# Kernel tuning notes

Hardware: AMD Instinct MI355X
Metric: run time of the kernel (lower is better)

## Reference

```python
import jax, jax.numpy as jnp
import numpy as np

M, K, N = 32768, 2048, 2048  # tokens, in_features, out_features
QMIN, QMAX = -128, 127


def setup_inputs() -> dict:
    key = jax.random.key(0)
    ks = jax.random.split(key, 7)
    x = jax.random.normal(ks[0], (M, K), dtype=jnp.float32).astype(jnp.float16)
    int_weight = jax.random.randint(ks[1], (N, K), QMIN, QMAX + 1, dtype=jnp.int32).astype(jnp.int8)
    # calibrated-looking asymmetric activation quant params (fp16 buffers, [num_steps]=1)
    act_delta = (jax.random.uniform(ks[2], (1,), dtype=jnp.float32) * 0.02 + 0.005).astype(jnp.float16)
    act_zp = jnp.round(jax.random.normal(ks[3], (1,), dtype=jnp.float32) * 8.0).astype(jnp.float16)
    # per-output-channel weight scales; fuse precomputed dequant buffers consistently
    w_delta = jax.random.uniform(ks[4], (N,), dtype=jnp.float32) * 0.002 + 1e-4
    act_times_weight_delta = (act_delta.astype(jnp.float32) * w_delta)[None, :]  # [1, N]
    w_row_sum = jnp.sum(int_weight.astype(jnp.float32), axis=1)  # [N]
    zp_times_weight_channel_sum = (act_zp.astype(jnp.float32) * w_row_sum * act_times_weight_delta[0])[None, :]  # [1, N]
    bias = jax.random.normal(ks[5], (N,), dtype=jnp.float32) * 0.02
    return {
        "input": x,
        "act_delta": act_delta,
        "act_zp": act_zp,
        "zp_times_weight_channel_sum": zp_times_weight_channel_sum,
        "act_times_weight_delta": act_times_weight_delta,
        "bias": bias,
        "int_weight": int_weight,
    }


def reference(input, act_delta, act_zp, zp_times_weight_channel_sum,
              act_times_weight_delta, bias, int_weight):
    # current_step == num_steps - 1 == 0
    delta = act_delta[0].astype(jnp.float32)
    zp = act_zp[0].astype(jnp.float32)
    atwd = act_times_weight_delta[0]            # [N] = act_delta * weight_delta
    zp_sum = zp_times_weight_channel_sum[0]     # [N] = zp * rowsum(W_int) * atwd
    # asymmetric int8 activation quantization: q = clip(round(x/delta + zp))
    q = jnp.clip(jnp.round(input.astype(jnp.float32) / delta + zp), QMIN, QMAX).astype(jnp.int8)
    # int8 GEMM with int32 accumulation: [M,K] x [K,N]
    acc = jnp.matmul(q.astype(jnp.int32), int_weight.astype(jnp.int32).T)
    # fused dequant + zero-point correction + bias, cast to fp16
    out = acc.astype(jnp.float32) * atwd - zp_sum + bias
    return out.astype(jnp.float16)
```

## Files before the change

### kernel.cpp

```cpp
#include <hip/hip_runtime.h>
#include <hip/hip_fp16.h>
#include <stdint.h>

typedef int i32x4 __attribute__((ext_vector_type(4)));

#define TM 128
#define TN 128
#define BK 64

__device__ __forceinline__ void gload_lds16(const void* g, void* l) {
  __builtin_amdgcn_global_load_lds(
      (const __attribute__((address_space(1))) unsigned int*)g,
      (__attribute__((address_space(3))) unsigned int*)l, 16, 0, 0);
}

__global__ __launch_bounds__(256) void quant_x_kernel(
    const float* __restrict__ x, const float* __restrict__ deltap,
    const float* __restrict__ zpp, int8_t* __restrict__ q, int n16) {
  int i = blockIdx.x * blockDim.x + threadIdx.x;
  if (i >= n16) return;
  const float delta = deltap[0];
  const float zp = zpp[0];
  const float4* src = (const float4*)x + (size_t)i * 4;
  int packed[4];
#pragma unroll
  for (int g = 0; g < 4; ++g) {
    float4 v = src[g];
    float f0 = fminf(127.f, fmaxf(-128.f, rintf(v.x / delta + zp)));
    float f1 = fminf(127.f, fmaxf(-128.f, rintf(v.y / delta + zp)));
    float f2 = fminf(127.f, fmaxf(-128.f, rintf(v.z / delta + zp)));
    float f3 = fminf(127.f, fmaxf(-128.f, rintf(v.w / delta + zp)));
    int q0 = (int)f0 & 255, q1 = (int)f1 & 255, q2 = (int)f2 & 255, q3 = (int)f3 & 255;
    packed[g] = q0 | (q1 << 8) | (q2 << 16) | (q3 << 24);
  }
  ((int4*)q)[i] = make_int4(packed[0], packed[1], packed[2], packed[3]);
}

__global__ __launch_bounds__(256) void pack_w_kernel(
    const int* __restrict__ w, int8_t* __restrict__ wp, int n16) {
  int i = blockIdx.x * blockDim.x + threadIdx.x;
  if (i >= n16) return;
  const int4* src = (const int4*)w + (size_t)i * 4;
  int packed[4];
#pragma unroll
  for (int g = 0; g < 4; ++g) {
    int4 v = src[g];
    packed[g] = (v.x & 255) | ((v.y & 255) << 8) | ((v.z & 255) << 16) | ((v.w & 255) << 24);
  }
  ((int4*)wp)[i] = make_int4(packed[0], packed[1], packed[2], packed[3]);
}

__global__ __launch_bounds__(256) void gemm_i8_kernel(
    const int8_t* __restrict__ Aq, const int8_t* __restrict__ Bw,
    const float* __restrict__ atwd, const float* __restrict__ zpws,
    const float* __restrict__ bias, float* __restrict__ out,
    int Mc, int Nc, int Kc) {
  __shared__ int8_t sA[TM * BK];
  __shared__ int8_t sB[TN * BK];
  const int bm = blockIdx.y;
  const int bn = blockIdx.x;
  const int t = threadIdx.x;
  const int lane = t & 63;
  const int wave = t >> 6;
  const int wr = wave >> 1;
  const int wc = wave & 1;
  const int fr = lane & 15;
  const int kc = lane >> 4;
  const size_t K = (size_t)Kc;

  i32x4 acc[4][4] = {};

  const int srow = t >> 2;
  const int scol = (t & 3) << 4;
  const int8_t* gA = Aq + (size_t)(bm * TM + srow) * K + scol;
  const int8_t* gB = Bw + (size_t)(bn * TN + srow) * K + scol;
  int8_t* lA = &sA[t * 16];
  int8_t* lB = &sB[t * 16];
  const size_t rowoff = (size_t)64 * K;

  for (int k0 = 0; k0 < Kc; k0 += BK) {
    gload_lds16(gA + k0, lA);
    gload_lds16(gA + k0 + rowoff, lA + 64 * BK);
    gload_lds16(gB + k0, lB);
    gload_lds16(gB + k0 + rowoff, lB + 64 * BK);
    __syncthreads();

    i32x4 af[4], bf[4];
#pragma unroll
    for (int i = 0; i < 4; ++i)
      af[i] = *(const i32x4*)&sA[(wr * 64 + i * 16 + fr) * BK + kc * 16];
#pragma unroll
    for (int j = 0; j < 4; ++j)
      bf[j] = *(const i32x4*)&sB[(wc * 64 + j * 16 + fr) * BK + kc * 16];

#pragma unroll
    for (int i = 0; i < 4; ++i)
#pragma unroll
      for (int j = 0; j < 4; ++j)
        acc[i][j] = __builtin_amdgcn_mfma_i32_16x16x64_i8(af[i], bf[j], acc[i][j], 0, 0, 0);

    __syncthreads();
  }

  const int r4 = (lane >> 4) << 2;
#pragma unroll
  for (int j = 0; j < 4; ++j) {
    const int cn = bn * TN + wc * 64 + j * 16 + fr;
    const float aw = atwd[cn];
    const float zs = zpws[cn];
    const float bs = bias[cn];
#pragma unroll
    for (int i = 0; i < 4; ++i) {
      const size_t rbase = (size_t)(bm * TM + wr * 64 + i * 16 + r4) * (size_t)Nc;
#pragma unroll
      for (int r = 0; r < 4; ++r) {
        float v = (float)acc[i][j][r] * aw - zs + bs;
        v = __half2float(__float2half(v));
        out[rbase + (size_t)r * Nc + cn] = v;
      }
    }
  }
}

extern "C" void kernel_launch(void* const* d_in, const int* in_sizes, int n_in,
                              void* d_out, int out_size, void* d_ws, size_t ws_size,
                              hipStream_t stream) {
  const float* x         = (const float*)d_in[0];
  const float* act_delta = (const float*)d_in[1];
  const float* act_zp    = (const float*)d_in[2];
  const float* zpws      = (const float*)d_in[3];
  const float* atwd      = (const float*)d_in[4];
  const float* bias      = (const float*)d_in[5];
  const int*   w32       = (const int*)d_in[6];
  float* out = (float*)d_out;

  const int N = in_sizes[5];
  const int K = in_sizes[6] / N;
  const int M = in_sizes[0] / K;

  int8_t* q  = (int8_t*)d_ws;
  int8_t* wp = q + (size_t)M * K;

  {
    int n16 = (M * K) / 16;
    quant_x_kernel<<<(n16 + 255) / 256, 256, 0, stream>>>(x, act_delta, act_zp, q, n16);
  }
  {
    int n16 = (N * K) / 16;
    pack_w_kernel<<<(n16 + 255) / 256, 256, 0, stream>>>(w32, wp, n16);
  }
  {
    dim3 grid(N / TN, M / TM);
    gemm_i8_kernel<<<grid, 256, 0, stream>>>(q, wp, atwd, zpws, bias, out, M, N, K);
  }
}
```

Before: 302.7 us.

## Rebuild int8 GEMM with 256x256 tiles, 4-slot LDS pipeline and swizzle

The GEMM moves from 128x128 tiles with a single LDS buffer to 256x256 tiles on 512 threads. A 4-slot LDS ring prefetches three K-steps ahead with explicit vmcnt waits, and MFMA phases are interleaved with the A and B staging. The change also adds an XOR swizzle on LDS columns to avoid bank conflicts, a 1D grid remapped for cache locality, and a reciprocal-multiply in the quantization kernel. The aim is to hide global-load latency and raise data reuse per tile. The cost is 128KB of LDS per block, which limits occupancy, plus hand-tuned wait counts that assume a particular load ordering.

New measurement: 271.1 us. 10.4% less time.

```diff
diff --git a/kernel.cpp b/kernel.cpp
--- a/kernel.cpp
+++ b/kernel.cpp
@@ -4,9 +4,12 @@
 
 typedef int i32x4 __attribute__((ext_vector_type(4)));
 
-#define TM 128
-#define TN 128
-#define BK 64
+#define BM 256
+#define BN 256
+#define BKB 64
+#define NSLOT 4
+#define SLOT_BYTES 32768
+#define THREADS 512
 
 __device__ __forceinline__ void gload_lds16(const void* g, void* l) {
   __builtin_amdgcn_global_load_lds(
@@ -19,17 +22,17 @@
     const float* __restrict__ zpp, int8_t* __restrict__ q, int n16) {
   int i = blockIdx.x * blockDim.x + threadIdx.x;
   if (i >= n16) return;
-  const float delta = deltap[0];
+  const float rdelta = 1.0f / deltap[0];
   const float zp = zpp[0];
   const float4* src = (const float4*)x + (size_t)i * 4;
   int packed[4];
 #pragma unroll
   for (int g = 0; g < 4; ++g) {
     float4 v = src[g];
-    float f0 = fminf(127.f, fmaxf(-128.f, rintf(v.x / delta + zp)));
-    float f1 = fminf(127.f, fmaxf(-128.f, rintf(v.y / delta + zp)));
-    float f2 = fminf(127.f, fmaxf(-128.f, rintf(v.z / delta + zp)));
-    float f3 = fminf(127.f, fmaxf(-128.f, rintf(v.w / delta + zp)));
+    float f0 = fminf(127.f, fmaxf(-128.f, rintf(fmaf(v.x, rdelta, zp))));
+    float f1 = fminf(127.f, fmaxf(-128.f, rintf(fmaf(v.y, rdelta, zp))));
+    float f2 = fminf(127.f, fmaxf(-128.f, rintf(fmaf(v.z, rdelta, zp))));
+    float f3 = fminf(127.f, fmaxf(-128.f, rintf(fmaf(v.w, rdelta, zp))));
     int q0 = (int)f0 & 255, q1 = (int)f1 & 255, q2 = (int)f2 & 255, q3 = (int)f3 & 255;
     packed[g] = q0 | (q1 << 8) | (q2 << 16) | (q3 << 24);
   }
@@ -50,71 +53,115 @@
   ((int4*)wp)[i] = make_int4(packed[0], packed[1], packed[2], packed[3]);
 }
 
-__global__ __launch_bounds__(256) void gemm_i8_kernel(
+__global__ __launch_bounds__(THREADS, 2) void gemm_i8_kernel(
     const int8_t* __restrict__ Aq, const int8_t* __restrict__ Bw,
     const float* __restrict__ atwd, const float* __restrict__ zpws,
     const float* __restrict__ bias, float* __restrict__ out,
     int Mc, int Nc, int Kc) {
-  __shared__ int8_t sA[TM * BK];
-  __shared__ int8_t sB[TN * BK];
-  const int bm = blockIdx.y;
-  const int bn = blockIdx.x;
-  const int t = threadIdx.x;
-  const int lane = t & 63;
-  const int wave = t >> 6;
-  const int wr = wave >> 1;
-  const int wc = wave & 1;
+  __shared__ int8_t lds[NSLOT * SLOT_BYTES];
+
+  const int nwg = gridDim.x;
+  int bid = blockIdx.x;
+  if ((nwg & 7) == 0) bid = (bid & 7) * (nwg >> 3) + (bid >> 3);
+  const int nbn = Nc / BN;
+  const int bm = bid / nbn;
+  const int bn = bid % nbn;
+
+  const int tid = threadIdx.x;
+  const size_t K = (size_t)Kc;
+  const int NT = Kc / BKB;
+
+  const int srow = tid >> 2;
+  const int c_log = (tid & 3) ^ ((tid >> 3) & 3);
+  const int8_t* gA = Aq + ((size_t)(bm * BM + srow)) * K + c_log * 16;
+  const int8_t* gB = Bw + ((size_t)(bn * BN + srow)) * K + c_log * 16;
+  const size_t half_off = (size_t)128 * K;
+  int8_t* ldst = &lds[tid * 16];
+
+  auto stageA = [&](int t, int h) {
+    gload_lds16(gA + (size_t)h * half_off + (size_t)t * BKB,
+                ldst + (t & 3) * SLOT_BYTES + h * 8192);
+  };
+  auto stageB = [&](int t, int h) {
+    gload_lds16(gB + (size_t)h * half_off + (size_t)t * BKB,
+                ldst + (t & 3) * SLOT_BYTES + 16384 + h * 8192);
+  };
+
+  const int lane = tid & 63;
+  const int wave = tid >> 6;
+  const int wr = wave >> 2;
+  const int wc = wave & 3;
   const int fr = lane & 15;
   const int kc = lane >> 4;
-  const size_t K = (size_t)Kc;
-
-  i32x4 acc[4][4] = {};
-
-  const int srow = t >> 2;
-  const int scol = (t & 3) << 4;
-  const int8_t* gA = Aq + (size_t)(bm * TM + srow) * K + scol;
-  const int8_t* gB = Bw + (size_t)(bn * TN + srow) * K + scol;
-  int8_t* lA = &sA[t * 16];
-  int8_t* lB = &sB[t * 16];
-  const size_t rowoff = (size_t)64 * K;
-
-  for (int k0 = 0; k0 < Kc; k0 += BK) {
-    gload_lds16(gA + k0, lA);
-    gload_lds16(gA + k0 + rowoff, lA + 64 * BK);
-    gload_lds16(gB + k0, lB);
-    gload_lds16(gB + k0 + rowoff, lB + 64 * BK);
-    __syncthreads();
-
-    i32x4 af[4], bf[4];
-#pragma unroll
-    for (int i = 0; i < 4; ++i)
-      af[i] = *(const i32x4*)&sA[(wr * 64 + i * 16 + fr) * BK + kc * 16];
+  const int coff = (kc ^ ((fr >> 1) & 3)) << 4;
+  const int aRow = wr * 128 + fr;
+  const int bRow = wc * 64 + fr;
+
+  i32x4 acc[8][4] = {};
+
+  stageA(0, 0); stageA(0, 1); stageB(0, 0); stageB(0, 1);
+  if (NT > 1) { stageA(1, 0); stageA(1, 1); stageB(1, 0); stageB(1, 1); }
+  if (NT > 2) { stageA(2, 0); stageA(2, 1); stageB(2, 0); stageB(2, 1); }
+  if (NT >= 3) asm volatile("s_waitcnt vmcnt(8)" ::: "memory");
+  else         asm volatile("s_waitcnt vmcnt(0)" ::: "memory");
+  __builtin_amdgcn_s_barrier();
+
+  for (int t = 0; t < NT; ++t) {
+    const int8_t* sA = &lds[(t & 3) * SLOT_BYTES];
+    const int8_t* sB = sA + 16384;
+    const bool pf = (t + 3 < NT);
+    i32x4 bfr[4], afr[4];
+
 #pragma unroll
     for (int j = 0; j < 4; ++j)
-      bf[j] = *(const i32x4*)&sB[(wc * 64 + j * 16 + fr) * BK + kc * 16];
-
+      bfr[j] = *(const i32x4*)&sB[(bRow + j * 16) * 64 + coff];
+#pragma unroll
+    for (int i = 0; i < 4; ++i)
+      afr[i] = *(const i32x4*)&sA[(aRow + i * 16) * 64 + coff];
+    if (pf) { stageA(t + 3, 0); stageA(t + 3, 1); }
+    __builtin_amdgcn_s_barrier();
+    asm volatile("s_waitcnt lgkmcnt(0)" ::: "memory");
+    __builtin_amdgcn_s_setprio(1);
 #pragma unroll
     for (int i = 0; i < 4; ++i)
 #pragma unroll
       for (int j = 0; j < 4; ++j)
-        acc[i][j] = __builtin_amdgcn_mfma_i32_16x16x64_i8(af[i], bf[j], acc[i][j], 0, 0, 0);
-
-    __syncthreads();
+        acc[i][j] = __builtin_amdgcn_mfma_i32_16x16x64_i8(afr[i], bfr[j], acc[i][j], 0, 0, 0);
+    __builtin_amdgcn_s_setprio(0);
+    __builtin_amdgcn_s_barrier();
+
+#pragma unroll
+    for (int i = 0; i < 4; ++i)
+      afr[i] = *(const i32x4*)&sA[(aRow + 64 + i * 16) * 64 + coff];
+    if (pf) { stageB(t + 3, 0); stageB(t + 3, 1); }
+    __builtin_amdgcn_s_barrier();
+    asm volatile("s_waitcnt lgkmcnt(0)" ::: "memory");
+    __builtin_amdgcn_s_setprio(1);
+#pragma unroll
+    for (int i = 0; i < 4; ++i)
+#pragma unroll
+      for (int j = 0; j < 4; ++j)
+        acc[4 + i][j] = __builtin_amdgcn_mfma_i32_16x16x64_i8(afr[i], bfr[j], acc[4 + i][j], 0, 0, 0);
+    __builtin_amdgcn_s_setprio(0);
+    if (t < NT - 3)       asm volatile("s_waitcnt vmcnt(8)" ::: "memory");
+    else if (t == NT - 3) asm volatile("s_waitcnt vmcnt(4)" ::: "memory");
+    else if (t == NT - 2) asm volatile("s_waitcnt vmcnt(0)" ::: "memory");
+    __builtin_amdgcn_s_barrier();
   }
 
   const int r4 = (lane >> 4) << 2;
 #pragma unroll
   for (int j = 0; j < 4; ++j) {
-    const int cn = bn * TN + wc * 64 + j * 16 + fr;
+    const int cn = bn * BN + wc * 64 + j * 16 + fr;
     const float aw = atwd[cn];
     const float zs = zpws[cn];
     const float bs = bias[cn];
 #pragma unroll
-    for (int i = 0; i < 4; ++i) {
-      const size_t rbase = (size_t)(bm * TM + wr * 64 + i * 16 + r4) * (size_t)Nc;
+    for (int mi = 0; mi < 8; ++mi) {
+      const size_t rbase = (size_t)(bm * BM + wr * 128 + mi * 16 + r4) * (size_t)Nc;
 #pragma unroll
       for (int r = 0; r < 4; ++r) {
-        float v = (float)acc[i][j][r] * aw - zs + bs;
+        float v = (float)acc[mi][j][r] * aw - zs + bs;
         v = __half2float(__float2half(v));
         out[rbase + (size_t)r * Nc + cn] = v;
       }
@@ -150,7 +197,7 @@
     pack_w_kernel<<<(n16 + 255) / 256, 256, 0, stream>>>(w32, wp, n16);
   }
   {
-    dim3 grid(N / TN, M / TM);
-    gemm_i8_kernel<<<grid, 256, 0, stream>>>(q, wp, atwd, zpws, bias, out, M, N, K);
-  }
-}
+    dim3 grid((M / BM) * (N / BN));
+    gemm_i8_kernel<<<grid, THREADS, 0, stream>>>(q, wp, atwd, zpws, bias, out, M, N, K);
+  }
+}
```
